# Kernel optimization log

Hardware: AMD Instinct MI355X
Metric: run time of the kernel (lower is better)

## Reference

```python
import jax, jax.numpy as jnp
import numpy as np

B, LQ, LK, D, H = 8, 512, 512, 512, 128

def setup_inputs() -> dict:
    key = jax.random.key(0)
    k1, k2, k3, k4, k5 = jax.random.split(key, 5)
    qs = jax.random.normal(k1, (B, LQ, D), dtype=jnp.float32)
    ks = jax.random.normal(k2, (B, LK, D), dtype=jnp.float32)
    # Dense kernels: flax Dense stores kernel as [in_features, out_features]
    Wq = jax.random.normal(k3, (D, H), dtype=jnp.float32) / np.sqrt(D)
    Wk = jax.random.normal(k4, (D, H), dtype=jnp.float32) / np.sqrt(D)
    wv = jax.random.normal(k5, (H,), dtype=jnp.float32) / np.sqrt(H)
    return {"qs": qs, "ks": ks, "Wq": Wq, "Wk": Wk, "wv": wv}

def reference(qs, ks, Wq, Wk, wv):
    # Project queries and keys into the shared hidden space: [B,Lq,H], [B,Lk,H]
    q = jnp.einsum("bqd,dh->bqh", qs, Wq)
    k = jnp.einsum("bkd,dh->bkh", ks, Wk)
    # Broadcast-add -> tanh -> linear reduce over H: scores [B,Lq,Lk]
    feats = jnp.tanh(q[:, :, None, :] + k[:, None, :, :])  # [B,Lq,Lk,H]
    return jnp.einsum("bqkh,h->bqk", feats, wv)
```

## Files before the change

### kernel.cpp

```cpp
#include <hip/hip_runtime.h>
#include <hip/hip_bf16.h>
#include <cstdint>

#define B_   8
#define LQ_  512
#define LK_  512
#define D_   512
#define H_   128

typedef __attribute__((ext_vector_type(8))) short  short8;
typedef __attribute__((ext_vector_type(4))) float  float4v;

#define TANH_C 2.8853900817779268f

__device__ __forceinline__ short bf16rne(float x) {
  uint32_t u = __float_as_uint(x);
  return (short)((u + 0x7fffu + ((u >> 16) & 1u)) >> 16);
}

__global__ __launch_bounds__(256) void prep_kernel(
    const float* __restrict__ Wq, const float* __restrict__ Wk,
    short* __restrict__ WqF, short* __restrict__ WkF) {
  int g = blockIdx.x * 256 + threadIdx.x;
  int m = g >> 13;
  int r = g & 8191;
  int l  = r & 63;
  int kb = (r >> 6) & 15;
  int nt = r >> 10;
  int col = nt * 16 + (l & 15);
  int k0  = kb * 32 + ((l >> 4) << 3);
  const float* W = m ? Wk : Wq;
  short8 f;
#pragma unroll
  for (int j = 0; j < 8; ++j) f[j] = bf16rne(W[(k0 + j) * H_ + col]);
  ((short8*)(m ? WkF : WqF))[r] = f;
}

__global__ __launch_bounds__(256) void proj_kernel(
    const float* __restrict__ qs, const float* __restrict__ ks,
    const short* __restrict__ WqF, const short* __restrict__ WkF,
    float* __restrict__ qp, float* __restrict__ kp) {
  int blk  = blockIdx.x;
  int wave = threadIdx.x >> 6;
  int l    = threadIdx.x & 63;
  int grow = blk * 16;
  int m    = (grow >= 4096) ? 1 : 0;
  int r0   = grow - (m ? 4096 : 0);
  const float*  A  = m ? ks : qs;
  const short8* BF = (const short8*)(m ? WkF : WqF);
  float* out = m ? kp : qp;

  float4v acc[2];
  acc[0] = (float4v){0.f, 0.f, 0.f, 0.f};
  acc[1] = (float4v){0.f, 0.f, 0.f, 0.f};

  int quad = l >> 4;
  int arow = r0 + (l & 15);
  const float* aptr = A + (size_t)arow * D_ + quad * 8;
  int t0 = wave * 2;

#pragma unroll 4
  for (int kb = 0; kb < 16; ++kb) {
    float4v a0 = *(const float4v*)(aptr + kb * 32);
    float4v a1 = *(const float4v*)(aptr + kb * 32 + 4);
    short8 af;
#pragma unroll
    for (int j = 0; j < 4; ++j) { af[j] = bf16rne(a0[j]); af[j + 4] = bf16rne(a1[j]); }
#pragma unroll
    for (int tt = 0; tt < 2; ++tt) {
      short8 bf = BF[((t0 + tt) * 16 + kb) * 64 + l];
      acc[tt] = __builtin_amdgcn_mfma_f32_16x16x32_bf16(af, bf, acc[tt], 0, 0, 0);
    }
  }

#pragma unroll
  for (int tt = 0; tt < 2; ++tt)
#pragma unroll
    for (int r = 0; r < 4; ++r) {
      int row = r0 + quad * 4 + r;
      int col = (t0 + tt) * 16 + (l & 15);
      out[(size_t)row * H_ + col] = __builtin_amdgcn_exp2f(acc[tt][r] * TANH_C);
    }
}

__global__ __launch_bounds__(256) void score_kernel(
    const float* __restrict__ qp, const float* __restrict__ kp,
    const float* __restrict__ wv, float* __restrict__ out) {
  __shared__ float qt[32 * 68];
  __shared__ float kt[32 * 68];

  int b = blockIdx.z, qtile = blockIdx.y, ktile = blockIdx.x;
  int t = threadIdx.x;
  int tx = t & 15, ty = t >> 4;

  const float* qbase = qp + (size_t)(b * LQ_ + qtile * 32) * H_;
  const float* kbase = kp + (size_t)(b * LK_ + ktile * 32) * H_;

  float W0 = 0.f;
  for (int h = 0; h < H_; ++h) W0 += wv[h];

  float4v acc4[2][2];
  const float4v ones = (float4v){1.f, 1.f, 1.f, 1.f};
#pragma unroll
  for (int i = 0; i < 2; ++i)
#pragma unroll
    for (int j = 0; j < 2; ++j) acc4[i][j] = (float4v){0.f, 0.f, 0.f, 0.f};

  int lr = t >> 4, lc = t & 15;

  for (int hc = 0; hc < 2; ++hc) {
    __syncthreads();
#pragma unroll
    for (int s = 0; s < 2; ++s) {
      int row = lr + 16 * s;
      *(float4v*)&qt[row * 68 + lc * 4] =
          *(const float4v*)&qbase[row * H_ + hc * 64 + lc * 4];
      *(float4v*)&kt[row * 68 + lc * 4] =
          *(const float4v*)&kbase[row * H_ + hc * 64 + lc * 4];
    }
    __syncthreads();

    for (int h0 = 0; h0 < 64; h0 += 4) {
      float4v qv[2], kv[2];
#pragma unroll
      for (int i = 0; i < 2; ++i) qv[i] = *(const float4v*)&qt[(ty + 16 * i) * 68 + h0];
#pragma unroll
      for (int j = 0; j < 2; ++j) kv[j] = *(const float4v*)&kt[(tx + 16 * j) * 68 + h0];
      const float* wp = wv + hc * 64 + h0;
      float4v w4 = (float4v){-2.f * wp[0], -2.f * wp[1], -2.f * wp[2], -2.f * wp[3]};

#pragma unroll
      for (int i = 0; i < 2; ++i)
#pragma unroll
        for (int j = 0; j < 2; ++j) {
          float4v den = __builtin_elementwise_fma(qv[i], kv[j], ones);
          float4v r;
          r[0] = __builtin_amdgcn_rcpf(den[0]);
          r[1] = __builtin_amdgcn_rcpf(den[1]);
          r[2] = __builtin_amdgcn_rcpf(den[2]);
          r[3] = __builtin_amdgcn_rcpf(den[3]);
          acc4[i][j] = __builtin_elementwise_fma(w4, r, acc4[i][j]);
        }
    }
  }

  size_t ob = (size_t)(b * LQ_ + qtile * 32) * LK_ + ktile * 32;
#pragma unroll
  for (int i = 0; i < 2; ++i)
#pragma unroll
    for (int j = 0; j < 2; ++j) {
      float4v a = acc4[i][j];
      out[ob + (size_t)(ty + 16 * i) * LK_ + tx + 16 * j] =
          W0 + ((a[0] + a[1]) + (a[2] + a[3]));
    }
}

extern "C" void kernel_launch(void* const* d_in, const int* in_sizes, int n_in,
                              void* d_out, int out_size, void* d_ws, size_t ws_size,
                              hipStream_t stream) {
  const float* qs = (const float*)d_in[0];
  const float* ks = (const float*)d_in[1];
  const float* Wq = (const float*)d_in[2];
  const float* Wk = (const float*)d_in[3];
  const float* wv = (const float*)d_in[4];
  float* out = (float*)d_out;

  char* ws = (char*)d_ws;
  short* WqF = (short*)ws;
  short* WkF = (short*)(ws + (128 << 10));
  float* qp  = (float*)(ws + (256 << 10));
  float* kp  = (float*)(ws + (256 << 10) + (2 << 20));

  prep_kernel<<<64, 256, 0, stream>>>(Wq, Wk, WqF, WkF);
  proj_kernel<<<512, 256, 0, stream>>>(qs, ks, WqF, WkF, qp, kp);
  score_kernel<<<dim3(16, 16, 8), 256, 0, stream>>>(qp, kp, wv, out);
}
```

Baseline: 112.0 us.

## Combine four reciprocals into one via common-denominator sum in score loop

The inner loop of the score kernel now sums four w/den terms over a shared common denominator, so it needs one rcp instead of four. Each output pays a few extra multiplies and FMAs in exchange, which relieves the transcendental unit. The per-block wv sum and the -2*wv scaling are moved into the prep kernel and read back from workspace. The product of four denominators can overflow or lose precision when exp2 values are large, which risks accuracy.

```diff
diff --git a/kernel.cpp b/kernel.cpp
--- a/kernel.cpp
+++ b/kernel.cpp
@@ -20,8 +20,19 @@
 
 __global__ __launch_bounds__(256) void prep_kernel(
     const float* __restrict__ Wq, const float* __restrict__ Wk,
-    short* __restrict__ WqF, short* __restrict__ WkF) {
+    const float* __restrict__ wv,
+    short* __restrict__ WqF, short* __restrict__ WkF,
+    float* __restrict__ w2, float* __restrict__ W0buf) {
   int g = blockIdx.x * 256 + threadIdx.x;
+  if (blockIdx.x == 0) {
+    int t = threadIdx.x;
+    if (t < H_) w2[t] = -2.0f * wv[t];
+    if (t == H_) {
+      float s = 0.f;
+      for (int h = 0; h < H_; ++h) s += wv[h];
+      W0buf[0] = s;
+    }
+  }
   int m = g >> 13;
   int r = g & 8191;
   int l  = r & 63;
@@ -85,7 +96,8 @@
 
 __global__ __launch_bounds__(256) void score_kernel(
     const float* __restrict__ qp, const float* __restrict__ kp,
-    const float* __restrict__ wv, float* __restrict__ out) {
+    const float* __restrict__ w2, const float* __restrict__ W0buf,
+    float* __restrict__ out) {
   __shared__ float qt[32 * 68];
   __shared__ float kt[32 * 68];
 
@@ -96,15 +108,14 @@
   const float* qbase = qp + (size_t)(b * LQ_ + qtile * 32) * H_;
   const float* kbase = kp + (size_t)(b * LK_ + ktile * 32) * H_;
 
-  float W0 = 0.f;
-  for (int h = 0; h < H_; ++h) W0 += wv[h];
+  float W0 = W0buf[0];
 
-  float4v acc4[2][2];
+  float accs[2][2];
   const float4v ones = (float4v){1.f, 1.f, 1.f, 1.f};
 #pragma unroll
   for (int i = 0; i < 2; ++i)
 #pragma unroll
-    for (int j = 0; j < 2; ++j) acc4[i][j] = (float4v){0.f, 0.f, 0.f, 0.f};
+    for (int j = 0; j < 2; ++j) accs[i][j] = 0.f;
 
   int lr = t >> 4, lc = t & 15;
 
@@ -126,20 +137,21 @@
       for (int i = 0; i < 2; ++i) qv[i] = *(const float4v*)&qt[(ty + 16 * i) * 68 + h0];
 #pragma unroll
       for (int j = 0; j < 2; ++j) kv[j] = *(const float4v*)&kt[(tx + 16 * j) * 68 + h0];
-      const float* wp = wv + hc * 64 + h0;
-      float4v w4 = (float4v){-2.f * wp[0], -2.f * wp[1], -2.f * wp[2], -2.f * wp[3]};
+      const float* wp = w2 + hc * 64 + h0;
+      float w0 = wp[0], w1 = wp[1], wA = wp[2], wB = wp[3];
 
 #pragma unroll
       for (int i = 0; i < 2; ++i)
 #pragma unroll
         for (int j = 0; j < 2; ++j) {
           float4v den = __builtin_elementwise_fma(qv[i], kv[j], ones);
-          float4v r;
-          r[0] = __builtin_amdgcn_rcpf(den[0]);
-          r[1] = __builtin_amdgcn_rcpf(den[1]);
-          r[2] = __builtin_amdgcn_rcpf(den[2]);
-          r[3] = __builtin_amdgcn_rcpf(den[3]);
-          acc4[i][j] = __builtin_elementwise_fma(w4, r, acc4[i][j]);
+          float d01 = den[0] * den[1];
+          float d23 = den[2] * den[3];
+          float n01 = fmaf(w1, den[0], w0 * den[1]);
+          float n23 = fmaf(wB, den[2], wA * den[3]);
+          float big = fmaf(n01, d23, n23 * d01);
+          float r   = __builtin_amdgcn_rcpf(d01 * d23);
+          accs[i][j] = fmaf(big, r, accs[i][j]);
         }
     }
   }
@@ -148,11 +160,8 @@
 #pragma unroll
   for (int i = 0; i < 2; ++i)
 #pragma unroll
-    for (int j = 0; j < 2; ++j) {
-      float4v a = acc4[i][j];
-      out[ob + (size_t)(ty + 16 * i) * LK_ + tx + 16 * j] =
-          W0 + ((a[0] + a[1]) + (a[2] + a[3]));
-    }
+    for (int j = 0; j < 2; ++j)
+      out[ob + (size_t)(ty + 16 * i) * LK_ + tx + 16 * j] = W0 + accs[i][j];
 }
 
 extern "C" void kernel_launch(void* const* d_in, const int* in_sizes, int n_in,
@@ -166,12 +175,14 @@
   float* out = (float*)d_out;
 
   char* ws = (char*)d_ws;
-  short* WqF = (short*)ws;
-  short* WkF = (short*)(ws + (128 << 10));
-  float* qp  = (float*)(ws + (256 << 10));
-  float* kp  = (float*)(ws + (256 << 10) + (2 << 20));
+  short* WqF  = (short*)ws;
+  short* WkF  = (short*)(ws + (128 << 10));
+  float* qp   = (float*)(ws + (256 << 10));
+  float* kp   = (float*)(ws + (256 << 10) + (2 << 20));
+  float* w2   = (float*)(ws + (256 << 10) + (4 << 20));
+  float* W0b  = (float*)(ws + (256 << 10) + (4 << 20) + 512);
 
-  prep_kernel<<<64, 256, 0, stream>>>(Wq, Wk, WqF, WkF);
+  prep_kernel<<<64, 256, 0, stream>>>(Wq, Wk, wv, WqF, WkF, w2, W0b);
   proj_kernel<<<512, 256, 0, stream>>>(qs, ks, WqF, WkF, qp, kp);
-  score_kernel<<<dim3(16, 16, 8), 256, 0, stream>>>(qp, kp, wv, out);
+  score_kernel<<<dim3(16, 16, 8), 256, 0, stream>>>(qp, kp, w2, W0b, out);
 }
```

After: 114.0 us. Within noise of the previous version (+1.8%).
